# Optimization experiments

Measured on AMD Instinct MI355X. Metric: run time of the kernel, lower is better.

Reference implementation:

```python
import jax, jax.numpy as jnp
import numpy as np

HIDDEN = 768
NUM_HEADS = 12
HEAD_DIM = HIDDEN // NUM_HEADS
B, S = 4, 2048


def setup_inputs() -> dict:
    key = jax.random.key(0)
    ks = jax.random.split(key, 10)
    scale = 1.0 / np.sqrt(HIDDEN)
    return {
        "hidden_states": jax.random.normal(ks[0], (B, S, HIDDEN), dtype=jnp.float32),
        "attention_mask": jnp.ones((B, S), dtype=jnp.float32),
        "Wq": jax.random.normal(ks[1], (HIDDEN, HIDDEN), dtype=jnp.float32) * scale,
        "bq": jnp.zeros((HIDDEN,), dtype=jnp.float32),
        "Wk": jax.random.normal(ks[2], (HIDDEN, HIDDEN), dtype=jnp.float32) * scale,
        "bk": jnp.zeros((HIDDEN,), dtype=jnp.float32),
        "Wv": jax.random.normal(ks[3], (HIDDEN, HIDDEN), dtype=jnp.float32) * scale,
        "bv": jnp.zeros((HIDDEN,), dtype=jnp.float32),
        "Wo": jax.random.normal(ks[4], (HIDDEN, HIDDEN), dtype=jnp.float32) * scale,
        "bo": jnp.zeros((HIDDEN,), dtype=jnp.float32),
    }


def reference(hidden_states, attention_mask, Wq, bq, Wk, bk, Wv, bv, Wo, bo):
    b, s, _ = hidden_states.shape
    # nn.Linear: x @ W.T + b  (W is [out, in])
    Q = hidden_states @ Wq.T + bq
    K = hidden_states @ Wk.T + bk
    V = hidden_states @ Wv.T + bv
    # [b, s, h*d] -> [b, h, s, d]
    Q = Q.reshape(b, s, NUM_HEADS, HEAD_DIM).transpose(0, 2, 1, 3)
    K = K.reshape(b, s, NUM_HEADS, HEAD_DIM).transpose(0, 2, 1, 3)
    V = V.reshape(b, s, NUM_HEADS, HEAD_DIM).transpose(0, 2, 1, 3)
    # scores: [b, h, s, s]
    scores = jnp.einsum("bhqd,bhkd->bhqk", Q, K) / jnp.sqrt(
        jnp.asarray(HEAD_DIM, dtype=Q.dtype))
    # mask: [b, s] -> additive bias broadcast over heads and query dim
    bias = (1.0 - attention_mask)[:, None, None, :] * -10000.0
    scores = scores + bias
    probs = jax.nn.softmax(scores, axis=-1)  # dropout p=0.0 -> identity
    context = jnp.einsum("bhqk,bhkd->bhqd", probs, V)
    context = context.transpose(0, 2, 1, 3).reshape(b, s, HIDDEN)
    return context @ Wo.T + bo
```

## Files before the change

### kernel.cpp

```cpp
#include <hip/hip_runtime.h>
#include <hip/hip_bf16.h>

#define SEQ   2048
#define NH    12
#define MTOK  8192

typedef __attribute__((ext_vector_type(8))) short short8;
typedef __attribute__((ext_vector_type(4))) short short4v;
typedef __attribute__((ext_vector_type(4))) float f32x4;

__device__ inline short f2bf(float x) {
  __hip_bfloat16 h = __float2bfloat16(x);
  return *(short*)&h;
}

#define GLL(gp, lp) __builtin_amdgcn_global_load_lds( \
    (const __attribute__((address_space(1))) void*)(gp), \
    (__attribute__((address_space(3))) void*)(lp), 16, 0, 0)

#define MFMA(a, b, c) __builtin_amdgcn_mfma_f32_16x16x32_bf16(a, b, c, 0, 0, 0)

#if !defined(__HIP_DEVICE_COMPILE__)
#define MFMA16(a, b, c) (c)
#elif __has_builtin(__builtin_amdgcn_mfma_f32_16x16x16bf16_1k)
#define MFMA16(a, b, c) __builtin_amdgcn_mfma_f32_16x16x16bf16_1k(a, b, c, 0, 0, 0)
#elif __has_builtin(__builtin_amdgcn_mfma_f32_16x16x16_bf16)
#define MFMA16(a, b, c) __builtin_amdgcn_mfma_f32_16x16x16_bf16(a, b, c, 0, 0, 0)
#else
#error "no 16x16x16 bf16 mfma builtin on device"
#endif

#if !defined(__HIP_DEVICE_COMPILE__)
#define EXP2(x) (x)
#elif __has_builtin(__builtin_amdgcn_exp2f)
#define EXP2(x) __builtin_amdgcn_exp2f(x)
#else
#define EXP2(x) __expf((x) * 0.6931471805599453f)
#endif

__device__ inline unsigned pack2bf(float a, float b) {
  unsigned ua = __float_as_uint(a) + 0x8000u;
  unsigned ub = __float_as_uint(b) + 0x8000u;
#if defined(__HIP_DEVICE_COMPILE__) && __has_builtin(__builtin_amdgcn_perm)
  return __builtin_amdgcn_perm(ub, ua, 0x07060302u);
#else
  return (ub & 0xFFFF0000u) | (ua >> 16);
#endif
}

union PackFrag {
  unsigned u[2];
  short4v s;
};

#define QSCALE 0.18033688011112042f
#define MBSCALE -14426.950408889634f

__global__ __launch_bounds__(256) void to_bf16(
    const float* __restrict__ in, short* __restrict__ out, int n4) {
  int i = blockIdx.x * 256 + threadIdx.x;
  if (i >= n4) return;
  float4 v = ((const float4*)in)[i];
  short4v o;
  o[0] = f2bf(v.x); o[1] = f2bf(v.y); o[2] = f2bf(v.z); o[3] = f2bf(v.w);
  ((short4v*)out)[i] = o;
}

__global__ __launch_bounds__(256) void conv_w(
    const float* __restrict__ Wq, const float* __restrict__ Wk,
    const float* __restrict__ Wv, const float* __restrict__ Wo,
    short* __restrict__ Wqkvb, short* __restrict__ Wob) {
  int idx = blockIdx.x * 256 + threadIdx.x;
  int r = idx / 192, c = (idx - r * 192) * 4;
  const float* src;
  short* dst;
  int rr;
  if (r < 768)       { src = Wq; rr = r;        dst = Wqkvb; }
  else if (r < 1536) { src = Wk; rr = r - 768;  dst = Wqkvb; }
  else if (r < 2304) { src = Wv; rr = r - 1536; dst = Wqkvb; }
  else               { src = Wo; rr = r - 2304; dst = Wob; r = rr; }
  float4 v = *(const float4*)&src[(size_t)rr * 768 + c];
  short4v o;
  o[0] = f2bf(v.x); o[1] = f2bf(v.y); o[2] = f2bf(v.z); o[3] = f2bf(v.w);
  *(short4v*)&dst[(size_t)r * 768 + c] = o;
}

__global__ __launch_bounds__(256) void maskbias(
    const float* __restrict__ mask, float* __restrict__ mb) {
  int i = blockIdx.x * 256 + threadIdx.x;
  if (i < MTOK) mb[i] = (1.f - mask[i]) * MBSCALE;
}

#define GEMM_BK64_LOOP(Aptr, Bptr)                                            \
  __shared__ __align__(16) short As[128 * 64];                                \
  __shared__ __align__(16) short Bs[128 * 64];                                \
  const int t = threadIdx.x;                                                  \
  const int wid = t >> 6, lane = t & 63, l15 = lane & 15, quad = lane >> 4;   \
  const int bm = blockIdx.x * 128, bn = blockIdx.y * 128;                     \
  const int mq = (wid & 1) * 64, nq = (wid >> 1) * 64;                        \
  const int srow8 = lane >> 3;           \
  const int schunk = lane & 7;                        \
  const int scol = (schunk ^ srow8) * 8;    \
  f32x4 acc[4][4] = {};                                                       \
  const short *gA[4], *gB[4];                                                 \
  _Pragma("unroll") for (int g = 0; g < 4; ++g) {                             \
    int row = wid * 32 + g * 8 + srow8;                                       \
    gA[g] = (Aptr) + (size_t)(bm + row) * 768 + scol;                         \
    gB[g] = (Bptr) + (size_t)(bn + row) * 768 + scol;                         \
  }                                                                           \
  for (int k0 = 0; k0 < 768; k0 += 64) {                                      \
    _Pragma("unroll") for (int g = 0; g < 4; ++g)                             \
      GLL(gA[g] + k0, &As[(wid * 32 + g * 8) * 64]);                          \
    _Pragma("unroll") for (int g = 0; g < 4; ++g)                             \
      GLL(gB[g] + k0, &Bs[(wid * 32 + g * 8) * 64]);                          \
    __syncthreads();                                                          \
    _Pragma("unroll") for (int ks = 0; ks < 2; ++ks) {                        \
      short8 a[4], b[4];                                                      \
      _Pragma("unroll") for (int mt = 0; mt < 4; ++mt)                        \
        a[mt] = *(const short8*)&As[(mq + mt * 16 + l15) * 64 +               \
                                    (((ks * 4 + quad) ^ (l15 & 7)) * 8)];     \
      _Pragma("unroll") for (int nt = 0; nt < 4; ++nt)                        \
        b[nt] = *(const short8*)&Bs[(nq + nt * 16 + l15) * 64 +               \
                                    (((ks * 4 + quad) ^ (l15 & 7)) * 8)];     \
      _Pragma("unroll") for (int mt = 0; mt < 4; ++mt)                        \
        _Pragma("unroll") for (int nt = 0; nt < 4; ++nt)                      \
          acc[mt][nt] = MFMA(a[mt], b[nt], acc[mt][nt]);                      \
    }                                                                         \
    __syncthreads();                                                          \
  }

__global__ __launch_bounds__(256) void gemm_qkv(
    const short* __restrict__ A, const short* __restrict__ B,
    const float* __restrict__ bq, const float* __restrict__ bk,
    const float* __restrict__ bv, short* __restrict__ Qb,
    short* __restrict__ Kb, short* __restrict__ Vt) {
  GEMM_BK64_LOOP(A, B)

  const int seg = bn >= 1536 ? 2 : (bn >= 768 ? 1 : 0);
  const float* bias = seg == 0 ? bq : (seg == 1 ? bk : bv);
  const int colbase = bn - seg * 768;

  if (seg < 2) {
    short* dst = seg == 0 ? Qb : Kb;
    const float sc = seg == 0 ? QSCALE : 1.f;
#pragma unroll
    for (int mt = 0; mt < 4; ++mt)
#pragma unroll
      for (int nt = 0; nt < 4; ++nt) {
        int col = colbase + nq + nt * 16 + l15;
        float bias_v = bias[col];
#pragma unroll
        for (int i = 0; i < 4; ++i) {
          int row = bm + mq + mt * 16 + quad * 4 + i;
          dst[(size_t)row * 768 + col] = f2bf((acc[mt][nt][i] + bias_v) * sc);
        }
      }
  } else {
#pragma unroll
    for (int mt = 0; mt < 4; ++mt) {
      int row0 = bm + mq + mt * 16 + quad * 4;
      int b_ = row0 >> 11, s = row0 & 2047;
#pragma unroll
      for (int nt = 0; nt < 4; ++nt) {
        int col = colbase + nq + nt * 16 + l15;
        float bias_v = bias[col];
        int h = col >> 6, d = col & 63;
        short4v pv;
#pragma unroll
        for (int i = 0; i < 4; ++i) pv[i] = f2bf(acc[mt][nt][i] + bias_v);
        *(short4v*)&Vt[(((size_t)b_ * NH + h) * 64 + d) * 2048 + s] = pv;
      }
    }
  }
}

__global__ __launch_bounds__(256) void gemm_out(
    const short* __restrict__ A, const short* __restrict__ B,
    const float* __restrict__ bias, float* __restrict__ C) {
  GEMM_BK64_LOOP(A, B)

#pragma unroll
  for (int mt = 0; mt < 4; ++mt)
#pragma unroll
    for (int nt = 0; nt < 4; ++nt) {
      int col = bn + nq + nt * 16 + l15;
      float bias_v = bias[col];
#pragma unroll
      for (int i = 0; i < 4; ++i) {
        int row = bm + mq + mt * 16 + quad * 4 + i;
        C[(size_t)row * 768 + col] = acc[mt][nt][i] + bias_v;
      }
    }
}

__global__ __launch_bounds__(256, 3) void attn_v7(
    const short* __restrict__ Qb, const short* __restrict__ Kb,
    const short* __restrict__ Vt, const float* __restrict__ maskb,
    short* __restrict__ Ctx) {
  __shared__ __align__(16) short Ks[64 * 64];
  __shared__ __align__(16) short Vs[64 * 64];
  const int t = threadIdx.x;
  const int w = t >> 6, lane = t & 63, l15 = lane & 15, quad = lane >> 4;
  const int bh = blockIdx.x, b = bh / NH, h = bh % NH;
  const int q0 = blockIdx.y * 128;

  short8 qa[2][2];
#pragma unroll
  for (int qt = 0; qt < 2; ++qt)
#pragma unroll
    for (int ks = 0; ks < 2; ++ks) {
      int row = b * 2048 + q0 + w * 32 + qt * 16 + l15;
      qa[qt][ks] = *(const short8*)&Qb[(size_t)row * 768 + h * 64 + ks * 32 + quad * 8];
    }

  f32x4 O[2][4] = {};
  f32x4 lacc[2] = {};
  short4v ones4;
#pragma unroll
  for (int j = 0; j < 4; ++j) ones4[j] = (short)0x3F80;

  const int r0 = w * 16 + (lane >> 3);
  const int pc = lane & 7;
  const int swz0 = (pc ^ (r0 & 7)) * 8;
  const int swz1 = (pc ^ ((r0 + 8) & 7)) * 8;
  const short* gK0 = Kb + (size_t)(b * 2048 + r0) * 768 + h * 64 + swz0;
  const short* gK1 = Kb + (size_t)(b * 2048 + r0 + 8) * 768 + h * 64 + swz1;
  const short* gV0 = Vt + ((size_t)bh * 64 + r0) * 2048 + swz0;
  const short* gV1 = Vt + ((size_t)bh * 64 + r0 + 8) * 2048 + swz1;
  const float* mb = maskb + b * 2048;
  const int rs = l15 & 7;

  for (int k0 = 0; k0 < SEQ; k0 += 64) {
    GLL(gK0 + (size_t)k0 * 768, &Ks[(w * 16) * 64]);
    GLL(gK1 + (size_t)k0 * 768, &Ks[(w * 16 + 8) * 64]);
    GLL(gV0 + k0, &Vs[(w * 16) * 64]);
    GLL(gV1 + k0, &Vs[(w * 16 + 8) * 64]);
    __syncthreads();

    f32x4 S[4][2] = {};
#pragma unroll
    for (int ks = 0; ks < 2; ++ks) {
      short8 kb[4];
#pragma unroll
      for (int kt = 0; kt < 4; ++kt)
        kb[kt] = *(const short8*)&Ks[(kt * 16 + l15) * 64 +
                                     (((ks * 4 + quad) ^ rs) * 8)];
#pragma unroll
      for (int kt = 0; kt < 4; ++kt) {
        S[kt][0] = MFMA(kb[kt], qa[0][ks], S[kt][0]);
        S[kt][1] = MFMA(kb[kt], qa[1][ks], S[kt][1]);
      }
    }

    short4v pb[4][2];
#pragma unroll
    for (int kt = 0; kt < 4; ++kt) {
      float4 mb4 = *(const float4*)&mb[k0 + kt * 16 + quad * 4];
#pragma unroll
      for (int qt = 0; qt < 2; ++qt) {
        float p0 = EXP2(S[kt][qt][0] + mb4.x);
        float p1 = EXP2(S[kt][qt][1] + mb4.y);
        float p2 = EXP2(S[kt][qt][2] + mb4.z);
        float p3 = EXP2(S[kt][qt][3] + mb4.w);
        PackFrag pf;
        pf.u[0] = pack2bf(p0, p1);
        pf.u[1] = pack2bf(p2, p3);
        pb[kt][qt] = pf.s;
      }
    }

#pragma unroll
    for (int kt = 0; kt < 4; ++kt) {
      lacc[0] = MFMA16(ones4, pb[kt][0], lacc[0]);
      lacc[1] = MFMA16(ones4, pb[kt][1], lacc[1]);
    }

#pragma unroll
    for (int kt = 0; kt < 4; ++kt) {
#pragma unroll
      for (int dt = 0; dt < 4; ++dt) {
        short4v av = *(const short4v*)&Vs[(dt * 16 + l15) * 64 +
            (((kt * 2 + (quad >> 1)) ^ rs) * 8) + (quad & 1) * 4];
        O[0][dt] = MFMA16(av, pb[kt][0], O[0][dt]);
        O[1][dt] = MFMA16(av, pb[kt][1], O[1][dt]);
      }
    }
    __syncthreads();
  }

#pragma unroll
  for (int qt = 0; qt < 2; ++qt) {
    float inv = 1.f / lacc[qt][0];
    int row = b * 2048 + q0 + w * 32 + qt * 16 + l15;
#pragma unroll
    for (int dt = 0; dt < 4; ++dt) {
      PackFrag pf;
      pf.u[0] = pack2bf(O[qt][dt][0] * inv, O[qt][dt][1] * inv);
      pf.u[1] = pack2bf(O[qt][dt][2] * inv, O[qt][dt][3] * inv);
      *(short4v*)&Ctx[(size_t)row * 768 + h * 64 + dt * 16 + quad * 4] = pf.s;
    }
  }
}

extern "C" void kernel_launch(void* const* d_in, const int* in_sizes, int n_in,
                              void* d_out, int out_size, void* d_ws,
                              size_t ws_size, hipStream_t stream) {
  const float* hs   = (const float*)d_in[0];
  const float* mask = (const float*)d_in[1];
  const float* Wq   = (const float*)d_in[2];
  const float* bq   = (const float*)d_in[3];
  const float* Wk   = (const float*)d_in[4];
  const float* bk   = (const float*)d_in[5];
  const float* Wv   = (const float*)d_in[6];
  const float* bv   = (const float*)d_in[7];
  const float* Wo   = (const float*)d_in[8];
  const float* bo   = (const float*)d_in[9];

  char* ws = (char*)d_ws;
  short* Xb    = (short*)(ws);
  short* Wqkvb = (short*)(ws + 12582912);
  short* Wob   = (short*)(ws + 16121856);
  short* Qb    = (short*)(ws + 17301504);
  short* Kb    = (short*)(ws + 29884416);
  short* Vtg   = (short*)(ws + 42467328);
  short* Ctxb  = (short*)(ws + 55050240);
  float* mbias = (float*)(ws + 67633152);

  to_bf16<<<6144, 256, 0, stream>>>(hs, Xb, 1572864);
  conv_w<<<2304, 256, 0, stream>>>(Wq, Wk, Wv, Wo, Wqkvb, Wob);
  maskbias<<<32, 256, 0, stream>>>(mask, mbias);

  gemm_qkv<<<dim3(64, 18), 256, 0, stream>>>(Xb, Wqkvb, bq, bk, bv,
                                             Qb, Kb, Vtg);
  attn_v7<<<dim3(48, 16), 256, 0, stream>>>(Qb, Kb, Vtg, mbias, Ctxb);
  gemm_out<<<dim3(64, 6), 256, 0, stream>>>(Ctxb, Wob, bo, (float*)d_out);
}
```

Before: 236.0 us.

## Double-buffer K/V tiles in attention and merge prep kernels into one launch

The attention kernel now keeps two LDS buffers for K and V. Each iteration prefetches the next tile with global_load_lds while computing on the current one, and one of the two barriers per iteration is removed. The three preprocessing kernels (activation cast, weight cast, mask bias) are merged into a single launch dispatched by block index, which saves two launch overheads. The extra buffers double attention LDS use, which could limit occupancy. The last iteration issues a wasted wraparound prefetch of tile 0.

```diff
diff --git a/kernel.cpp b/kernel.cpp
--- a/kernel.cpp
+++ b/kernel.cpp
@@ -56,39 +56,37 @@
 #define QSCALE 0.18033688011112042f
 #define MBSCALE -14426.950408889634f
 
-__global__ __launch_bounds__(256) void to_bf16(
-    const float* __restrict__ in, short* __restrict__ out, int n4) {
-  int i = blockIdx.x * 256 + threadIdx.x;
-  if (i >= n4) return;
-  float4 v = ((const float4*)in)[i];
-  short4v o;
-  o[0] = f2bf(v.x); o[1] = f2bf(v.y); o[2] = f2bf(v.z); o[3] = f2bf(v.w);
-  ((short4v*)out)[i] = o;
-}
-
-__global__ __launch_bounds__(256) void conv_w(
-    const float* __restrict__ Wq, const float* __restrict__ Wk,
-    const float* __restrict__ Wv, const float* __restrict__ Wo,
-    short* __restrict__ Wqkvb, short* __restrict__ Wob) {
-  int idx = blockIdx.x * 256 + threadIdx.x;
-  int r = idx / 192, c = (idx - r * 192) * 4;
-  const float* src;
-  short* dst;
-  int rr;
-  if (r < 768)       { src = Wq; rr = r;        dst = Wqkvb; }
-  else if (r < 1536) { src = Wk; rr = r - 768;  dst = Wqkvb; }
-  else if (r < 2304) { src = Wv; rr = r - 1536; dst = Wqkvb; }
-  else               { src = Wo; rr = r - 2304; dst = Wob; r = rr; }
-  float4 v = *(const float4*)&src[(size_t)rr * 768 + c];
-  short4v o;
-  o[0] = f2bf(v.x); o[1] = f2bf(v.y); o[2] = f2bf(v.z); o[3] = f2bf(v.w);
-  *(short4v*)&dst[(size_t)r * 768 + c] = o;
-}
-
-__global__ __launch_bounds__(256) void maskbias(
-    const float* __restrict__ mask, float* __restrict__ mb) {
-  int i = blockIdx.x * 256 + threadIdx.x;
-  if (i < MTOK) mb[i] = (1.f - mask[i]) * MBSCALE;
+__global__ __launch_bounds__(256) void prep(
+    const float* __restrict__ hs, const float* __restrict__ Wq,
+    const float* __restrict__ Wk, const float* __restrict__ Wv,
+    const float* __restrict__ Wo, const float* __restrict__ mask,
+    short* __restrict__ Xb, short* __restrict__ Wqkvb,
+    short* __restrict__ Wob, float* __restrict__ mbias) {
+  int bid = blockIdx.x;
+  if (bid < 6144) {
+    int i = bid * 256 + threadIdx.x;
+    float4 v = ((const float4*)hs)[i];
+    short4v o;
+    o[0] = f2bf(v.x); o[1] = f2bf(v.y); o[2] = f2bf(v.z); o[3] = f2bf(v.w);
+    ((short4v*)Xb)[i] = o;
+  } else if (bid < 6144 + 2304) {
+    int idx = (bid - 6144) * 256 + threadIdx.x;
+    int r = idx / 192, c = (idx - r * 192) * 4;
+    const float* src;
+    short* dst;
+    int rr;
+    if (r < 768)       { src = Wq; rr = r;        dst = Wqkvb; }
+    else if (r < 1536) { src = Wk; rr = r - 768;  dst = Wqkvb; }
+    else if (r < 2304) { src = Wv; rr = r - 1536; dst = Wqkvb; }
+    else               { src = Wo; rr = r - 2304; dst = Wob; r = rr; }
+    float4 v = *(const float4*)&src[(size_t)rr * 768 + c];
+    short4v o;
+    o[0] = f2bf(v.x); o[1] = f2bf(v.y); o[2] = f2bf(v.z); o[3] = f2bf(v.w);
+    *(short4v*)&dst[(size_t)r * 768 + c] = o;
+  } else {
+    int i = (bid - 6144 - 2304) * 256 + threadIdx.x;
+    if (i < MTOK) mbias[i] = (1.f - mask[i]) * MBSCALE;
+  }
 }
 
 #define GEMM_BK64_LOOP(Aptr, Bptr)                                            \
@@ -98,9 +96,9 @@
   const int wid = t >> 6, lane = t & 63, l15 = lane & 15, quad = lane >> 4;   \
   const int bm = blockIdx.x * 128, bn = blockIdx.y * 128;                     \
   const int mq = (wid & 1) * 64, nq = (wid >> 1) * 64;                        \
-  const int srow8 = lane >> 3;           \
-  const int schunk = lane & 7;                        \
-  const int scol = (schunk ^ srow8) * 8;    \
+  const int srow8 = lane >> 3;                                                \
+  const int schunk = lane & 7;                                                \
+  const int scol = (schunk ^ srow8) * 8;                                      \
   f32x4 acc[4][4] = {};                                                       \
   const short *gA[4], *gB[4];                                                 \
   _Pragma("unroll") for (int g = 0; g < 4; ++g) {                             \
@@ -193,12 +191,12 @@
     }
 }
 
-__global__ __launch_bounds__(256, 3) void attn_v7(
+__global__ __launch_bounds__(256, 3) void attn_v8(
     const short* __restrict__ Qb, const short* __restrict__ Kb,
     const short* __restrict__ Vt, const float* __restrict__ maskb,
     short* __restrict__ Ctx) {
-  __shared__ __align__(16) short Ks[64 * 64];
-  __shared__ __align__(16) short Vs[64 * 64];
+  __shared__ __align__(16) short Ks[2][64 * 64];
+  __shared__ __align__(16) short Vs[2][64 * 64];
   const int t = threadIdx.x;
   const int w = t >> 6, lane = t & 63, l15 = lane & 15, quad = lane >> 4;
   const int bh = blockIdx.x, b = bh / NH, h = bh % NH;
@@ -230,12 +228,23 @@
   const float* mb = maskb + b * 2048;
   const int rs = l15 & 7;
 
-  for (int k0 = 0; k0 < SEQ; k0 += 64) {
-    GLL(gK0 + (size_t)k0 * 768, &Ks[(w * 16) * 64]);
-    GLL(gK1 + (size_t)k0 * 768, &Ks[(w * 16 + 8) * 64]);
-    GLL(gV0 + k0, &Vs[(w * 16) * 64]);
-    GLL(gV1 + k0, &Vs[(w * 16 + 8) * 64]);
+  GLL(gK0, &Ks[0][(w * 16) * 64]);
+  GLL(gK1, &Ks[0][(w * 16 + 8) * 64]);
+  GLL(gV0, &Vs[0][(w * 16) * 64]);
+  GLL(gV1, &Vs[0][(w * 16 + 8) * 64]);
+
+  for (int ti = 0; ti < 32; ++ti) {
+    const int cur = ti & 1;
+    const int k0 = ti * 64;
     __syncthreads();
+
+    {
+      const size_t kn = (size_t)(((ti + 1) & 31) * 64);
+      GLL(gK0 + kn * 768, &Ks[1 - cur][(w * 16) * 64]);
+      GLL(gK1 + kn * 768, &Ks[1 - cur][(w * 16 + 8) * 64]);
+      GLL(gV0 + kn, &Vs[1 - cur][(w * 16) * 64]);
+      GLL(gV1 + kn, &Vs[1 - cur][(w * 16 + 8) * 64]);
+    }
 
     f32x4 S[4][2] = {};
 #pragma unroll
@@ -243,8 +252,8 @@
       short8 kb[4];
 #pragma unroll
       for (int kt = 0; kt < 4; ++kt)
-        kb[kt] = *(const short8*)&Ks[(kt * 16 + l15) * 64 +
-                                     (((ks * 4 + quad) ^ rs) * 8)];
+        kb[kt] = *(const short8*)&Ks[cur][(kt * 16 + l15) * 64 +
+                                         (((ks * 4 + quad) ^ rs) * 8)];
 #pragma unroll
       for (int kt = 0; kt < 4; ++kt) {
         S[kt][0] = MFMA(kb[kt], qa[0][ks], S[kt][0]);
@@ -279,13 +288,12 @@
     for (int kt = 0; kt < 4; ++kt) {
 #pragma unroll
       for (int dt = 0; dt < 4; ++dt) {
-        short4v av = *(const short4v*)&Vs[(dt * 16 + l15) * 64 +
+        short4v av = *(const short4v*)&Vs[cur][(dt * 16 + l15) * 64 +
             (((kt * 2 + (quad >> 1)) ^ rs) * 8) + (quad & 1) * 4];
         O[0][dt] = MFMA16(av, pb[kt][0], O[0][dt]);
         O[1][dt] = MFMA16(av, pb[kt][1], O[1][dt]);
       }
     }
-    __syncthreads();
   }
 
 #pragma unroll
@@ -326,12 +334,10 @@
   short* Ctxb  = (short*)(ws + 55050240);
   float* mbias = (float*)(ws + 67633152);
 
-  to_bf16<<<6144, 256, 0, stream>>>(hs, Xb, 1572864);
-  conv_w<<<2304, 256, 0, stream>>>(Wq, Wk, Wv, Wo, Wqkvb, Wob);
-  maskbias<<<32, 256, 0, stream>>>(mask, mbias);
-
+  prep<<<8480, 256, 0, stream>>>(hs, Wq, Wk, Wv, Wo, mask,
+                                 Xb, Wqkvb, Wob, mbias);
   gemm_qkv<<<dim3(64, 18), 256, 0, stream>>>(Xb, Wqkvb, bq, bk, bv,
                                              Qb, Kb, Vtg);
-  attn_v7<<<dim3(48, 16), 256, 0, stream>>>(Qb, Kb, Vtg, mbias, Ctxb);
+  attn_v8<<<dim3(48, 16), 256, 0, stream>>>(Qb, Kb, Vtg, mbias, Ctxb);
   gemm_out<<<dim3(64, 6), 256, 0, stream>>>(Ctxb, Wob, bo, (float*)d_out);
 }
```

After: 229.1 us. -2.9%, faster.
